# Optimization experiments

Hardware: AMD Instinct MI355X
Metric: run time of the kernel (lower is better)

## Reference

```python
import jax, jax.numpy as jnp
from jax import lax
import numpy as np

KSIZE = 3        # matching kernel size
RATE = 2         # downsample rate; raw kernel = 2*RATE = 4
FUSE_K = 3       # fusion (diagonal-sum) kernel size
SOFTMAX_SCALE = 10.0
EPS = 1e-4


def extract_patches(x, k, s, pad):
    """im2col: x [B,C,H,W] -> patches [B, L, C, k, k], L = oH*oW (row-major),
    matching torch.nn.Unfold ordering after the view/permute in the source."""
    B, C, H, W = x.shape
    xp = jnp.pad(x, ((0, 0), (0, 0), (pad, pad), (pad, pad)))
    Hp, Wp = H + 2 * pad, W + 2 * pad
    oH = (Hp - k) // s + 1
    oW = (Wp - k) // s + 1
    cols = []
    for i in range(k):
        for j in range(k):
            cols.append(xp[:, :, i:i + (oH - 1) * s + 1:s, j:j + (oW - 1) * s + 1:s])
    p = jnp.stack(cols, axis=0).reshape(k, k, B, C, oH, oW)
    return p.transpose(2, 4, 5, 3, 0, 1).reshape(B, oH * oW, C, k, k)


def fuse_diag(y, k):
    """conv2d with identity (eye(k)) kernel, 'same' padding == sum of diagonal shifts."""
    r = k // 2
    n0, n1 = y.shape
    yp = jnp.pad(y, r)
    return sum(yp[r + d:r + d + n0, r + d:r + d + n1] for d in range(-r, r + 1))


def _per_sample(xi, wi, raw_wi, mi):
    # xi: [C,Hs,Ws] downsampled foreground; wi: [L,C,3,3] bg patches;
    # raw_wi: [L,C,4,4] raw bg patches; mi: [L] patch validity mask
    C, Hs, Ws = xi.shape
    L = wi.shape[0]
    # L2-normalize each background patch (EPS added per-element inside the sum, as in source)
    wi_norm = jnp.sqrt(jnp.sum(wi * wi + EPS, axis=(1, 2, 3), keepdims=True))
    wn = (wi / wi_norm).reshape(L, -1)                      # [L, C*9]
    # correlation scores: conv2d(xi, wi_normed, pad=1) expressed as a GEMM over im2col patches
    fp = extract_patches(xi[None], KSIZE, 1, KSIZE // 2)[0].reshape(L, -1)  # [L_f, C*9]
    yi = wn @ fp.T                                          # [L_b, L_f]
    # fusion trick: identity-kernel conv along both diagonal orientations
    yi = fuse_diag(yi, FUSE_K)
    yi = yi.reshape(Hs, Ws, Hs, Ws).transpose(1, 0, 3, 2).reshape(L, L)
    yi = fuse_diag(yi, FUSE_K)
    yi = yi.reshape(Ws, Hs, Ws, Hs).transpose(1, 0, 3, 2)
    yi = yi.reshape(L, Hs, Ws)
    m = mi[:, None, None]
    yi = jax.nn.softmax(yi * m * SOFTMAX_SCALE, axis=0) * m  # softmax over bg-patch axis
    # transposed conv reconstruction with raw 4x4 patches, stride=RATE, padding=1
    k = 2 * RATE
    w_t = jnp.flip(raw_wi, (2, 3)).transpose(1, 0, 2, 3)     # [C, L, 4, 4] OIHW
    out = lax.conv_general_dilated(
        yi[None], w_t, window_strides=(1, 1),
        padding=[(k - 1 - 1, k - 1 - 1)] * 2, lhs_dilation=(RATE, RATE),
        dimension_numbers=('NCHW', 'OIHW', 'NCHW'))[0] / 4.0  # [C, H, W]
    return out


def setup_inputs() -> dict:
    key = jax.random.key(0)
    k1, k2 = jax.random.split(key)
    B, C, H, W = 4, 128, 96, 96
    b = jax.random.normal(k1, (B, C, H, W), jnp.float32)
    f = jax.random.normal(k2, (B, C, H, W), jnp.float32)
    mask = jnp.ones((B, 1, H, W), jnp.float32)
    return {"b": b, "f": f, "mask": mask}


def reference(b, f, mask):
    B, C, H, W = b.shape
    k_raw = 2 * RATE
    # raw patches from full-res background: k=4, stride=2, pad=1 (get_pad 'valid')
    raw_w = extract_patches(b, k_raw, RATE, 1)               # [B, L, C, 4, 4]
    # nearest downsample by RATE (F.interpolate nearest, scale 1/rate)
    fs = f[:, :, ::RATE, ::RATE]
    bs = b[:, :, ::RATE, ::RATE]
    Hs, Ws = fs.shape[2], fs.shape[3]
    w = extract_patches(bs, KSIZE, 1, KSIZE // 2)            # [B, L, C, 3, 3]
    ms = mask.shape[3] // Ws
    m_small = mask[:, :, ::ms, ::ms]                         # [B, 1, Hs, Ws]
    m = extract_patches(m_small, KSIZE, 1, KSIZE // 2)       # [B, L, 1, 3, 3]
    mm = (jnp.mean(m, axis=(2, 3, 4)) == 1.0).astype(jnp.float32)  # [B, L]
    y = jax.vmap(_per_sample)(fs, w, raw_w, mm)              # [B, C, H, W]
    return y
```

## Files before the change

### kernel.cpp

```cpp
#include <hip/hip_runtime.h>
#include <hip/hip_bf16.h>
#include <math.h>

#define NS   4
#define CH   128
#define HW   96
#define GS   48
#define LL   2304
#define CKN  2048
#define SCALE 10.0f
#define EPSSUM 0.1152f
#define PCH2 32
#define NCH2 72

#define S_IN  ((size_t)CH * HW * HW)
#define S_MK  ((size_t)HW * HW)
#define S_BS  ((size_t)CH * LL)
#define S_PM  ((size_t)NCH2 * LL)
#define S_BUF ((size_t)LL * LL)
#define S_W2  ((size_t)CKN * LL)
#define S_AT  ((size_t)LL * LL)

typedef __attribute__((ext_vector_type(8))) short short8;
typedef __attribute__((ext_vector_type(4))) float float4v;

#define GLDS16(gptr, lptr) \
    __builtin_amdgcn_global_load_lds((const __attribute__((address_space(1))) void*)(gptr), \
        (__attribute__((address_space(3))) void*)(lptr), 16, 0, 0)

__device__ __forceinline__ float4 ld4(const float* p) { return *reinterpret_cast<const float4*>(p); }


__global__ __launch_bounds__(256) void k_stage(const float* __restrict__ b, const float* __restrict__ f,
                                               float* __restrict__ bs_c, float* __restrict__ fs_c) {
    int s = blockIdx.z;
    b += s * S_IN; f += s * S_IN; bs_c += s * S_BS; fs_c += s * S_BS;
    int c  = blockIdx.y;
    int rs = blockIdx.x * 256 + threadIdx.x;
    int r = rs / GS, ss = rs % GS;
    int src = c * HW * HW + (2 * r) * HW + 2 * ss;
    bs_c[c * LL + rs] = b[src];
    fs_c[c * LL + rs] = f[src];
}

__global__ __launch_bounds__(256) void k_ssq(const float* __restrict__ bs_c, float* __restrict__ ssq) {
    int s = blockIdx.z;
    bs_c += s * S_BS; ssq += (size_t)s * LL;
    int rs = blockIdx.x * 256 + threadIdx.x;
    int c0 = blockIdx.y * 32;
    float acc = 0.f;
    for (int c = c0; c < c0 + 32; ++c) { float v = bs_c[c * LL + rs]; acc += v * v; }
    atomicAdd(&ssq[rs], acc);
}

__global__ __launch_bounds__(256) void k_norm_mm(const float* __restrict__ ssq, const float* __restrict__ mk,
                                                 float* __restrict__ invn, float* __restrict__ mmv) {
    int sI = blockIdx.z;
    ssq += (size_t)sI * LL; mk += sI * S_MK; invn += (size_t)sI * LL; mmv += (size_t)sI * LL;
    int p = blockIdx.x * 256 + threadIdx.x;
    int ph = p / GS, pw = p % GS;
    float acc = EPSSUM;
    float msum = 0.f;
    for (int di = -1; di <= 1; ++di)
        for (int dj = -1; dj <= 1; ++dj) {
            int r = ph + di, s = pw + dj;
            if (r >= 0 && r < GS && s >= 0 && s < GS) {
                acc  += ssq[r * GS + s];
                msum += mk[(2 * r) * HW + 2 * s];
            }
        }
    invn[p] = 1.0f / sqrtf(acc);
    mmv[p]  = (msum / 9.0f == 1.0f) ? 1.0f : 0.0f;
}

__global__ __launch_bounds__(256) void k_w2T(const float* __restrict__ b, __hip_bfloat16* __restrict__ W2T) {
    int sI = blockIdx.z;
    b += sI * S_IN; W2T += sI * S_W2;
    int ck = blockIdx.y;
    int p  = blockIdx.x * 256 + threadIdx.x;
    int c = ck >> 4, dy = (ck >> 2) & 3, dx = ck & 3;
    int ph = p / GS, pw = p % GS;
    int r = 2 * ph + dy - 1, s = 2 * pw + dx - 1;
    float v = 0.f;
    if (r >= 0 && r < HW && s >= 0 && s < HW) v = b[c * HW * HW + r * HW + s];
    W2T[(size_t)ck * LL + p] = __float2bfloat16(v);
}

__global__ __launch_bounds__(256) void k_split_T(const float* __restrict__ bs_c, const float* __restrict__ fs_c,
                                                 float* __restrict__ bufB) {
    __shared__ float tile[32][33];
    int z = blockIdx.z;
    int s = z >> 1, sel = z & 1;
    const float* X = (sel ? fs_c : bs_c) + s * S_BS;
    __hip_bfloat16* base = (__hip_bfloat16*)(bufB + s * S_BUF);
    __hip_bfloat16* hi = base + (size_t)sel * 2 * LL * CH;
    __hip_bfloat16* lo = hi + (size_t)LL * CH;
    int r0 = blockIdx.x * 32, c0 = blockIdx.y * 32;
    int tx = threadIdx.x & 31, ty = threadIdx.x >> 5;
#pragma unroll
    for (int j = 0; j < 4; ++j)
        tile[ty + 8 * j][tx] = X[(size_t)(c0 + ty + 8 * j) * LL + r0 + tx];
    __syncthreads();
#pragma unroll
    for (int j = 0; j < 4; ++j) {
        int rl = ty + 8 * j, cl = tx;
        float v = tile[cl][rl];
        __hip_bfloat16 h = __float2bfloat16(v);
        float resid = v - __bfloat162float(h);
        hi[(size_t)(r0 + rl) * CH + c0 + cl] = h;
        lo[(size_t)(r0 + rl) * CH + c0 + cl] = __float2bfloat16(resid);
    }
}

__global__ __launch_bounds__(256) void gemm1_mfma(const float* __restrict__ bufB, float* __restrict__ bufA) {
    __shared__ __hip_bfloat16 sAh[128 * 32];
    __shared__ __hip_bfloat16 sAl[128 * 32];
    __shared__ __hip_bfloat16 sBh[128 * 32];
    __shared__ __hip_bfloat16 sBl[128 * 32];
    int sI = blockIdx.z;
    const __hip_bfloat16* base = (const __hip_bfloat16*)(bufB + sI * S_BUF);
    const __hip_bfloat16* Ahi = base;
    const __hip_bfloat16* Alo = Ahi + (size_t)LL * CH;
    const __hip_bfloat16* Bhi = Alo + (size_t)LL * CH;
    const __hip_bfloat16* Blo = Bhi + (size_t)LL * CH;
    float* C = bufA + sI * S_BUF;

    int t = threadIdx.x, lane = t & 63, w = t >> 6;
    int wr = w >> 1, wc = w & 1;
    int m0 = blockIdx.y * 128, n0 = blockIdx.x * 128;

    float4v acc[4][4];
#pragma unroll
    for (int i = 0; i < 4; ++i)
#pragma unroll
        for (int j = 0; j < 4; ++j) acc[i][j] = (float4v){0.f, 0.f, 0.f, 0.f};

    for (int k0 = 0; k0 < 128; k0 += 32) {
#pragma unroll
        for (int it = 0; it < 2; ++it) {
            int chunk = it * 256 + w * 64 + lane;
            int row = chunk >> 2, ps = chunk & 3;
            int pd = ps ^ (row & 3);
            size_t ga = (size_t)(m0 + row) * 128 + k0 + pd * 8;
            size_t gb = (size_t)(n0 + row) * 128 + k0 + pd * 8;
            GLDS16(Ahi + ga, (char*)sAh + (size_t)chunk * 16);
            GLDS16(Alo + ga, (char*)sAl + (size_t)chunk * 16);
            GLDS16(Bhi + gb, (char*)sBh + (size_t)chunk * 16);
            GLDS16(Blo + gb, (char*)sBl + (size_t)chunk * 16);
        }
        __syncthreads();

        int lrow = lane & 15, part = lane >> 4;
        int sw = part ^ (lrow & 3);
        short8 ah[4], al[4], bh[4], bl[4];
#pragma unroll
        for (int i = 0; i < 4; ++i) {
            int slot = (wr * 64 + i * 16 + lrow) * 4 + sw;
            ah[i] = *reinterpret_cast<const short8*>(sAh + (size_t)slot * 8);
            al[i] = *reinterpret_cast<const short8*>(sAl + (size_t)slot * 8);
        }
#pragma unroll
        for (int j = 0; j < 4; ++j) {
            int slot = (wc * 64 + j * 16 + lrow) * 4 + sw;
            bh[j] = *reinterpret_cast<const short8*>(sBh + (size_t)slot * 8);
            bl[j] = *reinterpret_cast<const short8*>(sBl + (size_t)slot * 8);
        }
#pragma unroll
        for (int i = 0; i < 4; ++i)
#pragma unroll
            for (int j = 0; j < 4; ++j) {
                acc[i][j] = __builtin_amdgcn_mfma_f32_16x16x32_bf16(ah[i], bh[j], acc[i][j], 0, 0, 0);
                acc[i][j] = __builtin_amdgcn_mfma_f32_16x16x32_bf16(ah[i], bl[j], acc[i][j], 0, 0, 0);
                acc[i][j] = __builtin_amdgcn_mfma_f32_16x16x32_bf16(al[i], bh[j], acc[i][j], 0, 0, 0);
            }
        __syncthreads();
    }

    int col = lane & 15, rbase = (lane >> 4) * 4;
#pragma unroll
    for (int i = 0; i < 4; ++i)
#pragma unroll
        for (int j = 0; j < 4; ++j)
#pragma unroll
            for (int r = 0; r < 4; ++r) {
                int m = m0 + wr * 64 + i * 16 + rbase + r;
                int n = n0 + wc * 64 + j * 16 + col;
                C[(size_t)m * LL + n] = acc[i][j][r];
            }
}

__global__ __launch_bounds__(256) void gemm2_mfma(const __hip_bfloat16* __restrict__ attnT,
                                                  const __hip_bfloat16* __restrict__ W2T,
                                                  float* __restrict__ bufA) {
    __shared__ __hip_bfloat16 As[128 * 32];
    __shared__ __hip_bfloat16 Bs[128 * 32];
    int sI = blockIdx.z;
    const __hip_bfloat16* A = attnT + sI * S_AT;
    const __hip_bfloat16* B = W2T + sI * S_W2;
    __hip_bfloat16* C = (__hip_bfloat16*)(bufA + sI * S_BUF);

    int t = threadIdx.x;
    int lane = t & 63, w = t >> 6;
    int wr = w >> 1, wc = w & 1;
    int m0 = blockIdx.y * 128, n0 = blockIdx.x * 128;

    float4v acc[4][4];
#pragma unroll
    for (int i = 0; i < 4; ++i)
#pragma unroll
        for (int j = 0; j < 4; ++j) acc[i][j] = (float4v){0.f, 0.f, 0.f, 0.f};

    for (int k0 = 0; k0 < LL; k0 += 32) {
#pragma unroll
        for (int it = 0; it < 2; ++it) {
            int chunk = it * 256 + w * 64 + lane;
            int row = chunk >> 2, ps = chunk & 3;
            int pd = ps ^ (row & 3);
            const __hip_bfloat16* ga = A + (size_t)(m0 + row) * LL + k0 + pd * 8;
            const __hip_bfloat16* gb = B + (size_t)(n0 + row) * LL + k0 + pd * 8;
            GLDS16(ga, (char*)As + (size_t)chunk * 16);
            GLDS16(gb, (char*)Bs + (size_t)chunk * 16);
        }
        __syncthreads();

        int lrow = lane & 15, part = lane >> 4;
        int sw = part ^ (lrow & 3);
        short8 afrag[4], bfrag[4];
#pragma unroll
        for (int i = 0; i < 4; ++i) {
            int slot = (wr * 64 + i * 16 + lrow) * 4 + sw;
            afrag[i] = *reinterpret_cast<const short8*>(As + (size_t)slot * 8);
        }
#pragma unroll
        for (int j = 0; j < 4; ++j) {
            int slot = (wc * 64 + j * 16 + lrow) * 4 + sw;
            bfrag[j] = *reinterpret_cast<const short8*>(Bs + (size_t)slot * 8);
        }
#pragma unroll
        for (int i = 0; i < 4; ++i)
#pragma unroll
            for (int j = 0; j < 4; ++j)
                acc[i][j] = __builtin_amdgcn_mfma_f32_16x16x32_bf16(afrag[i], bfrag[j], acc[i][j], 0, 0, 0);
        __syncthreads();
    }

    int col = lane & 15, rbase = (lane >> 4) * 4;
#pragma unroll
    for (int i = 0; i < 4; ++i)
#pragma unroll
        for (int j = 0; j < 4; ++j)
#pragma unroll
            for (int r = 0; r < 4; ++r) {
                int m = m0 + wr * 64 + i * 16 + rbase + r;
                int n = n0 + wc * 64 + j * 16 + col;
                C[(size_t)m * CKN + n] = __float2bfloat16(acc[i][j][r]);
            }
}

__global__ __launch_bounds__(192) void k_corr_v4(const float* __restrict__ bufA, const float* __restrict__ invn,
                                                 float* __restrict__ bufB) {
    int sI = blockIdx.z;
    const float* D = bufA + sI * S_BUF;
    float* yi = bufB + sI * S_BUF;
    invn += (size_t)sI * LL;

    int p  = blockIdx.y;
    int qi = blockIdx.x * 192 + threadIdx.x;
    int q4 = qi * 4;
    int qh = q4 / GS, qw0 = q4 % GS;
    int ph = p / GS, pw = p % GS;

    float4 acc = {0.f, 0.f, 0.f, 0.f};
#pragma unroll
    for (int di = -1; di <= 1; ++di) {
        int rp = ph + di, tq = qh + di;
        if (rp < 0 || rp >= GS || tq < 0 || tq >= GS) continue;
        int r0 = rp * GS + pw;
        int c0 = tq * GS + qw0;
        {
            float4 Cc = ld4(D + (size_t)r0 * LL + c0);
            acc.x += Cc.x; acc.y += Cc.y; acc.z += Cc.z; acc.w += Cc.w;
        }
        if (pw > 0) {
            const float* rowm = D + (size_t)(r0 - 1) * LL;
            float4 L  = ld4(rowm + (qw0 > 0 ? c0 - 4 : c0));
            float4 Cm = ld4(rowm + c0);
            acc.x += (qw0 > 0 ? L.w : 0.f);
            acc.y += Cm.x; acc.z += Cm.y; acc.w += Cm.z;
        }
        if (pw < GS - 1) {
            const float* rowp = D + (size_t)(r0 + 1) * LL;
            float4 Cp = ld4(rowp + c0);
            float4 R  = ld4(rowp + (qw0 < GS - 4 ? c0 + 4 : c0));
            acc.x += Cp.y; acc.y += Cp.z; acc.z += Cp.w;
            acc.w += (qw0 < GS - 4 ? R.x : 0.f);
        }
    }
    float inv = invn[p];
    float4 outv = {inv * acc.x, inv * acc.y, inv * acc.z, inv * acc.w};
    *reinterpret_cast<float4*>(yi + (size_t)p * LL + q4) = outv;
}

__global__ __launch_bounds__(192) void k_fuse1_v4(const float* __restrict__ bufB, float* __restrict__ bufA) {
    int sI = blockIdx.z;
    const float* yi = bufB + sI * S_BUF;
    float* S1 = bufA + sI * S_BUF;
    int a  = blockIdx.y;
    int bi = blockIdx.x * 192 + threadIdx.x;
    int b4 = bi * 4;

    float4 acc = ld4(yi + (size_t)a * LL + b4);
    if (a > 0) {
        const float* rowm = yi + (size_t)(a - 1) * LL;
        float4 L  = ld4(rowm + (b4 > 0 ? b4 - 4 : b4));
        float4 Cm = ld4(rowm + b4);
        acc.x += (b4 > 0 ? L.w : 0.f);
        acc.y += Cm.x; acc.z += Cm.y; acc.w += Cm.z;
    }
    if (a < LL - 1) {
        const float* rowp = yi + (size_t)(a + 1) * LL;
        float4 Cp = ld4(rowp + b4);
        float4 R  = ld4(rowp + (b4 < LL - 4 ? b4 + 4 : b4));
        acc.x += Cp.y; acc.y += Cp.z; acc.z += Cp.w;
        acc.w += (b4 < LL - 4 ? R.x : 0.f);
    }
    *reinterpret_cast<float4*>(S1 + (size_t)a * LL + b4) = acc;
}

__device__ __forceinline__ int gmap(int x) { int hi = x / GS; int lo = x - hi * GS; return lo * GS + hi; }

__global__ __launch_bounds__(256) void k_fuse2_sm(const float* __restrict__ bufA, const float* __restrict__ mmv,
                                                  float* __restrict__ bufB,
                                                  float* __restrict__ pmax, float* __restrict__ psum) {
    int sI = blockIdx.z;
    const float* S1 = bufA + sI * S_BUF;
    float* S2 = bufB + sI * S_BUF;
    mmv += (size_t)sI * LL; pmax += sI * S_PM; psum += sI * S_PM;
    int q = blockIdx.x * 256 + threadIdx.x;
    int qh = q / GS, qw = q % GS;
    int b0 = qw * GS + qh;
    int p0 = blockIdx.y * PCH2;
    float mx = -1e30f, sm = 0.f;
    for (int i = 0; i < PCH2; ++i) {
        int p = p0 + i;
        int ph = p / GS, pw = p % GS;
        int a0 = pw * GS + ph;
        float s = 0.f;
#pragma unroll
        for (int e = -1; e <= 1; ++e) {
            int ae = a0 + e, be = b0 + e;
            if (ae >= 0 && ae < LL && be >= 0 && be < LL)
                s += S1[(size_t)gmap(ae) * LL + gmap(be)];
        }
        S2[(size_t)p * LL + q] = s;
        float lg = (mmv[p] != 0.f) ? SCALE * s : 0.f;
        float nm = fmaxf(mx, lg);
        sm = sm * __expf(mx - nm) + __expf(lg - nm);
        mx = nm;
    }
    pmax[blockIdx.y * LL + q] = mx;
    psum[blockIdx.y * LL + q] = sm;
}

__global__ __launch_bounds__(256) void k_sm2(const float* __restrict__ pmax, const float* __restrict__ psum,
                                             float* __restrict__ Mq, float* __restrict__ Dq) {
    __shared__ float red[4][64];
    int sI = blockIdx.z;
    pmax += sI * S_PM; psum += sI * S_PM; Mq += (size_t)sI * LL; Dq += (size_t)sI * LL;
    int t = threadIdx.x;
    int ql = t & 63, g = t >> 6;
    int q = blockIdx.x * 64 + ql;
    float mx = -1e30f;
    for (int ch = g * 18; ch < g * 18 + 18; ++ch) mx = fmaxf(mx, pmax[(size_t)ch * LL + q]);
    red[g][ql] = mx;
    __syncthreads();
    float mall = fmaxf(fmaxf(red[0][ql], red[1][ql]), fmaxf(red[2][ql], red[3][ql]));
    float sm = 0.f;
    for (int ch = g * 18; ch < g * 18 + 18; ++ch)
        sm += psum[(size_t)ch * LL + q] * __expf(pmax[(size_t)ch * LL + q] - mall);
    __syncthreads();
    red[g][ql] = sm;
    __syncthreads();
    if (g == 0) {
        Mq[q] = mall;
        Dq[q] = (red[0][ql] + red[1][ql]) + (red[2][ql] + red[3][ql]);
    }
}

__global__ __launch_bounds__(256) void k_sm3T(const float* __restrict__ bufB, const float* __restrict__ mmv,
                                              const float* __restrict__ Mq, const float* __restrict__ Dq,
                                              __hip_bfloat16* __restrict__ attnT) {
    __shared__ float tile[32][33];
    int sI = blockIdx.z;
    const float* S2 = bufB + sI * S_BUF;
    mmv += (size_t)sI * LL; Mq += (size_t)sI * LL; Dq += (size_t)sI * LL; attnT += sI * S_AT;
    int tx = threadIdx.x & 31, ty = threadIdx.x >> 5;
    int p0 = blockIdx.y * 32, q0 = blockIdx.x * 32;
    int q = q0 + tx;
    float mq = Mq[q], dq = Dq[q];
#pragma unroll
    for (int j = 0; j < 4; ++j) {
        int p = p0 + ty + 8 * j;
        float v = S2[(size_t)p * LL + q];
        float attn = (mmv[p] != 0.f) ? __expf(SCALE * v - mq) / dq : 0.f;
        tile[ty + 8 * j][tx] = attn;
    }
    __syncthreads();
#pragma unroll
    for (int j = 0; j < 4; ++j) {
        int qq = q0 + ty + 8 * j;
        attnT[(size_t)qq * LL + p0 + tx] = __float2bfloat16(tile[tx][ty + 8 * j]);
    }
}

__global__ __launch_bounds__(256) void k_out(const float* __restrict__ bufA, float* __restrict__ out) {
    int sI = blockIdx.z;
    const __hip_bfloat16* Z = (const __hip_bfloat16*)(bufA + sI * S_BUF);
    out += sI * S_IN;
    int c  = blockIdx.y;
    int yx = blockIdx.x * 256 + threadIdx.x;
    int y = yx / HW, x = yx % HW;
    int u = y >> 1, a = y & 1, v = x >> 1, w = x & 1;
    int qh1 = u + a - 1, qh2 = u + a, qw1 = v + w - 1, qw2 = v + w;
    int cb = c * 16;
    float s = 0.f;
    if (qh1 >= 0) {
        if (qw1 >= 0)  s += __bfloat162float(Z[(size_t)(qh1 * GS + qw1) * CKN + cb + (3 - a) * 4 + (3 - w)]);
        if (qw2 < GS)  s += __bfloat162float(Z[(size_t)(qh1 * GS + qw2) * CKN + cb + (3 - a) * 4 + (1 - w)]);
    }
    if (qh2 < GS) {
        if (qw1 >= 0)  s += __bfloat162float(Z[(size_t)(qh2 * GS + qw1) * CKN + cb + (1 - a) * 4 + (3 - w)]);
        if (qw2 < GS)  s += __bfloat162float(Z[(size_t)(qh2 * GS + qw2) * CKN + cb + (1 - a) * 4 + (1 - w)]);
    }
    out[(size_t)c * HW * HW + yx] = 0.25f * s;
}


extern "C" void kernel_launch(void* const* d_in, const int* in_sizes, int n_in,
                              void* d_out, int out_size, void* d_ws, size_t ws_size,
                              hipStream_t stream) {
    const float* b_all = (const float*)d_in[0];
    const float* f_all = (const float*)d_in[1];
    const float* m_all = (const float*)d_in[2];
    float* out = (float*)d_out;
    float* ws  = (float*)d_ws;

    const size_t perF = 2 * S_BS + 5 * (size_t)LL + 2 * S_PM + 2 * S_BUF + S_W2 / 2 + S_AT / 2;
    const size_t perB = perF * sizeof(float);
    int nb = (ws_size >= NS * perB) ? NS : ((ws_size >= 2 * perB) ? 2 : 1);

    size_t off = 0;
    float* bs_c = ws + off; off += nb * S_BS;
    float* fs_c = ws + off; off += nb * S_BS;
    float* ssq  = ws + off; off += nb * (size_t)LL;
    float* invn = ws + off; off += nb * (size_t)LL;
    float* mmv  = ws + off; off += nb * (size_t)LL;
    float* Mq   = ws + off; off += nb * (size_t)LL;
    float* Dq   = ws + off; off += nb * (size_t)LL;
    float* pmax = ws + off; off += nb * S_PM;
    float* psum = ws + off; off += nb * S_PM;
    float* bufA = ws + off; off += nb * S_BUF;
    float* bufB = ws + off; off += nb * S_BUF;
    __hip_bfloat16* W2T   = (__hip_bfloat16*)(ws + off); off += nb * S_W2 / 2;
    __hip_bfloat16* attnT = (__hip_bfloat16*)(ws + off); off += nb * S_AT / 2;

    for (int s0 = 0; s0 < NS; s0 += nb) {
        const float* b  = b_all + s0 * S_IN;
        const float* f  = f_all + s0 * S_IN;
        const float* mk = m_all + s0 * S_MK;
        float* outp = out + s0 * S_IN;

        hipMemsetAsync(ssq, 0, nb * LL * sizeof(float), stream);
        k_stage    <<<dim3(9, CH, nb), 256, 0, stream>>>(b, f, bs_c, fs_c);
        k_ssq      <<<dim3(9, 4, nb), 256, 0, stream>>>(bs_c, ssq);
        k_norm_mm  <<<dim3(9, 1, nb), 256, 0, stream>>>(ssq, mk, invn, mmv);
        k_w2T      <<<dim3(9, CKN, nb), 256, 0, stream>>>(b, W2T);
        k_split_T  <<<dim3(72, 4, 2 * nb), 256, 0, stream>>>(bs_c, fs_c, bufB);

        gemm1_mfma <<<dim3(18, 18, nb), 256, 0, stream>>>(bufB, bufA);
        k_corr_v4  <<<dim3(3, LL, nb), 192, 0, stream>>>(bufA, invn, bufB);
        k_fuse1_v4 <<<dim3(3, LL, nb), 192, 0, stream>>>(bufB, bufA);
        k_fuse2_sm <<<dim3(9, NCH2, nb), 256, 0, stream>>>(bufA, mmv, bufB, pmax, psum);

        k_sm2      <<<dim3(36, 1, nb), 256, 0, stream>>>(pmax, psum, Mq, Dq);
        k_sm3T     <<<dim3(72, 72, nb), 256, 0, stream>>>(bufB, mmv, Mq, Dq, attnT);

        gemm2_mfma <<<dim3(CKN / 128, LL / 128, nb), 256, 0, stream>>>(attnT, W2T, bufA);
        k_out      <<<dim3(36, CH, nb), 256, 0, stream>>>(bufA, outp);
    }
}
```

Baseline: 550.9 us.

## Fuse first diagonal fusion pass into second and transpose gemm2 output layout

Removes the separate k_fuse1 kernel by computing the first diagonal sum inline inside k_fuse2_sm, which now reads nine neighbours of the correlation matrix directly instead of three from an intermediate buffer. This avoids writing and re-reading one full LL×LL fp32 buffer per sample, at the cost of three times more scattered gathers in the fused kernel. Separately, gemm2 swaps its operands so the output is stored channel-major ([CKN, LL]), and k_out now indexes along the spatial dimension, which should make neighbouring threads read adjacent addresses. Buffer roles are swapped to match.

```diff
diff --git a/kernel.cpp b/kernel.cpp
--- a/kernel.cpp
+++ b/kernel.cpp
@@ -189,15 +189,15 @@
             }
 }
 
-__global__ __launch_bounds__(256) void gemm2_mfma(const __hip_bfloat16* __restrict__ attnT,
-                                                  const __hip_bfloat16* __restrict__ W2T,
-                                                  float* __restrict__ bufA) {
+__global__ __launch_bounds__(256) void gemm2_mfma(const __hip_bfloat16* __restrict__ W2T_,
+                                                  const __hip_bfloat16* __restrict__ attnT_,
+                                                  float* __restrict__ bufB) {
     __shared__ __hip_bfloat16 As[128 * 32];
     __shared__ __hip_bfloat16 Bs[128 * 32];
     int sI = blockIdx.z;
-    const __hip_bfloat16* A = attnT + sI * S_AT;
-    const __hip_bfloat16* B = W2T + sI * S_W2;
-    __hip_bfloat16* C = (__hip_bfloat16*)(bufA + sI * S_BUF);
+    const __hip_bfloat16* A = W2T_ + sI * S_W2;
+    const __hip_bfloat16* B = attnT_ + sI * S_AT;
+    __hip_bfloat16* C = (__hip_bfloat16*)(bufB + sI * S_BUF);
 
     int t = threadIdx.x;
     int lane = t & 63, w = t >> 6;
@@ -253,7 +253,7 @@
             for (int r = 0; r < 4; ++r) {
                 int m = m0 + wr * 64 + i * 16 + rbase + r;
                 int n = n0 + wc * 64 + j * 16 + col;
-                C[(size_t)m * CKN + n] = __float2bfloat16(acc[i][j][r]);
+                C[(size_t)m * LL + n] = __float2bfloat16(acc[i][j][r]);
             }
 }
 
@@ -301,40 +301,14 @@
     *reinterpret_cast<float4*>(yi + (size_t)p * LL + q4) = outv;
 }
 
-__global__ __launch_bounds__(192) void k_fuse1_v4(const float* __restrict__ bufB, float* __restrict__ bufA) {
+__device__ __forceinline__ int gmap(int x) { int hi = x / GS; int lo = x - hi * GS; return lo * GS + hi; }
+
+__global__ __launch_bounds__(256) void k_fuse2_sm(const float* __restrict__ bufB, const float* __restrict__ mmv,
+                                                  float* __restrict__ bufA,
+                                                  float* __restrict__ pmax, float* __restrict__ psum) {
     int sI = blockIdx.z;
     const float* yi = bufB + sI * S_BUF;
-    float* S1 = bufA + sI * S_BUF;
-    int a  = blockIdx.y;
-    int bi = blockIdx.x * 192 + threadIdx.x;
-    int b4 = bi * 4;
-
-    float4 acc = ld4(yi + (size_t)a * LL + b4);
-    if (a > 0) {
-        const float* rowm = yi + (size_t)(a - 1) * LL;
-        float4 L  = ld4(rowm + (b4 > 0 ? b4 - 4 : b4));
-        float4 Cm = ld4(rowm + b4);
-        acc.x += (b4 > 0 ? L.w : 0.f);
-        acc.y += Cm.x; acc.z += Cm.y; acc.w += Cm.z;
-    }
-    if (a < LL - 1) {
-        const float* rowp = yi + (size_t)(a + 1) * LL;
-        float4 Cp = ld4(rowp + b4);
-        float4 R  = ld4(rowp + (b4 < LL - 4 ? b4 + 4 : b4));
-        acc.x += Cp.y; acc.y += Cp.z; acc.z += Cp.w;
-        acc.w += (b4 < LL - 4 ? R.x : 0.f);
-    }
-    *reinterpret_cast<float4*>(S1 + (size_t)a * LL + b4) = acc;
-}
-
-__device__ __forceinline__ int gmap(int x) { int hi = x / GS; int lo = x - hi * GS; return lo * GS + hi; }
-
-__global__ __launch_bounds__(256) void k_fuse2_sm(const float* __restrict__ bufA, const float* __restrict__ mmv,
-                                                  float* __restrict__ bufB,
-                                                  float* __restrict__ pmax, float* __restrict__ psum) {
-    int sI = blockIdx.z;
-    const float* S1 = bufA + sI * S_BUF;
-    float* S2 = bufB + sI * S_BUF;
+    float* S2 = bufA + sI * S_BUF;
     mmv += (size_t)sI * LL; pmax += sI * S_PM; psum += sI * S_PM;
     int q = blockIdx.x * 256 + threadIdx.x;
     int qh = q / GS, qw = q % GS;
@@ -349,8 +323,14 @@
 #pragma unroll
         for (int e = -1; e <= 1; ++e) {
             int ae = a0 + e, be = b0 + e;
-            if (ae >= 0 && ae < LL && be >= 0 && be < LL)
-                s += S1[(size_t)gmap(ae) * LL + gmap(be)];
+            if (ae < 0 || ae >= LL || be < 0 || be >= LL) continue;
+            int A = gmap(ae), B = gmap(be);
+#pragma unroll
+            for (int d = -1; d <= 1; ++d) {
+                int Ad = A + d, Bd = B + d;
+                if (Ad >= 0 && Ad < LL && Bd >= 0 && Bd < LL)
+                    s += yi[(size_t)Ad * LL + Bd];
+            }
         }
         S2[(size_t)p * LL + q] = s;
         float lg = (mmv[p] != 0.f) ? SCALE * s : 0.f;
@@ -387,12 +367,12 @@
     }
 }
 
-__global__ __launch_bounds__(256) void k_sm3T(const float* __restrict__ bufB, const float* __restrict__ mmv,
+__global__ __launch_bounds__(256) void k_sm3T(const float* __restrict__ S2buf, const float* __restrict__ mmv,
                                               const float* __restrict__ Mq, const float* __restrict__ Dq,
                                               __hip_bfloat16* __restrict__ attnT) {
     __shared__ float tile[32][33];
     int sI = blockIdx.z;
-    const float* S2 = bufB + sI * S_BUF;
+    const float* S2 = S2buf + sI * S_BUF;
     mmv += (size_t)sI * LL; Mq += (size_t)sI * LL; Dq += (size_t)sI * LL; attnT += sI * S_AT;
     int tx = threadIdx.x & 31, ty = threadIdx.x >> 5;
     int p0 = blockIdx.y * 32, q0 = blockIdx.x * 32;
@@ -413,9 +393,9 @@
     }
 }
 
-__global__ __launch_bounds__(256) void k_out(const float* __restrict__ bufA, float* __restrict__ out) {
-    int sI = blockIdx.z;
-    const __hip_bfloat16* Z = (const __hip_bfloat16*)(bufA + sI * S_BUF);
+__global__ __launch_bounds__(256) void k_out(const float* __restrict__ bufB, float* __restrict__ out) {
+    int sI = blockIdx.z;
+    const __hip_bfloat16* Z = (const __hip_bfloat16*)(bufB + sI * S_BUF);
     out += sI * S_IN;
     int c  = blockIdx.y;
     int yx = blockIdx.x * 256 + threadIdx.x;
@@ -425,12 +405,12 @@
     int cb = c * 16;
     float s = 0.f;
     if (qh1 >= 0) {
-        if (qw1 >= 0)  s += __bfloat162float(Z[(size_t)(qh1 * GS + qw1) * CKN + cb + (3 - a) * 4 + (3 - w)]);
-        if (qw2 < GS)  s += __bfloat162float(Z[(size_t)(qh1 * GS + qw2) * CKN + cb + (3 - a) * 4 + (1 - w)]);
+        if (qw1 >= 0)  s += __bfloat162float(Z[(size_t)(cb + (3 - a) * 4 + (3 - w)) * LL + qh1 * GS + qw1]);
+        if (qw2 < GS)  s += __bfloat162float(Z[(size_t)(cb + (3 - a) * 4 + (1 - w)) * LL + qh1 * GS + qw2]);
     }
     if (qh2 < GS) {
-        if (qw1 >= 0)  s += __bfloat162float(Z[(size_t)(qh2 * GS + qw1) * CKN + cb + (1 - a) * 4 + (3 - w)]);
-        if (qw2 < GS)  s += __bfloat162float(Z[(size_t)(qh2 * GS + qw2) * CKN + cb + (1 - a) * 4 + (1 - w)]);
+        if (qw1 >= 0)  s += __bfloat162float(Z[(size_t)(cb + (1 - a) * 4 + (3 - w)) * LL + qh2 * GS + qw1]);
+        if (qw2 < GS)  s += __bfloat162float(Z[(size_t)(cb + (1 - a) * 4 + (1 - w)) * LL + qh2 * GS + qw2]);
     }
     out[(size_t)c * HW * HW + yx] = 0.25f * s;
 }
@@ -479,13 +459,12 @@
 
         gemm1_mfma <<<dim3(18, 18, nb), 256, 0, stream>>>(bufB, bufA);
         k_corr_v4  <<<dim3(3, LL, nb), 192, 0, stream>>>(bufA, invn, bufB);
-        k_fuse1_v4 <<<dim3(3, LL, nb), 192, 0, stream>>>(bufB, bufA);
-        k_fuse2_sm <<<dim3(9, NCH2, nb), 256, 0, stream>>>(bufA, mmv, bufB, pmax, psum);
+        k_fuse2_sm <<<dim3(9, NCH2, nb), 256, 0, stream>>>(bufB, mmv, bufA, pmax, psum);
 
         k_sm2      <<<dim3(36, 1, nb), 256, 0, stream>>>(pmax, psum, Mq, Dq);
-        k_sm3T     <<<dim3(72, 72, nb), 256, 0, stream>>>(bufB, mmv, Mq, Dq, attnT);
-
-        gemm2_mfma <<<dim3(CKN / 128, LL / 128, nb), 256, 0, stream>>>(attnT, W2T, bufA);
-        k_out      <<<dim3(36, CH, nb), 256, 0, stream>>>(bufA, outp);
-    }
-}
+        k_sm3T     <<<dim3(72, 72, nb), 256, 0, stream>>>(bufA, mmv, Mq, Dq, attnT);
+
+        gemm2_mfma <<<dim3(LL / 128, CKN / 128, nb), 256, 0, stream>>>(W2T, attnT, bufB);
+        k_out      <<<dim3(36, CH, nb), 256, 0, stream>>>(bufB, outp);
+    }
+}
```

After: 587.4 us. 1.07x slower.
